# Kernel tuning notes

Measured on AMD Instinct MI355X. Metric: run time of the kernel, lower is better.

Reference implementation:

```python
import jax, jax.numpy as jnp
import numpy as np
from jax import lax

C = 128; HEADS = 16; HD = 8; EPS = 1e-5

def _conv3x3(x, w):
    return lax.conv_general_dilated(x, w, (1, 1), 'SAME', dimension_numbers=('NCHW', 'OIHW', 'NCHW'))

def _cbr3(x, w, g, b):
    # Conv3x3 + BatchNorm(eval, running stats folded -> per-channel affine) + ReLU
    return jax.nn.relu(_conv3x3(x, w) * g[:, None, None] + b[:, None, None])

def _cbr1(x, w, g, b):
    y = jnp.einsum('bchw,oc->bohw', x, w)
    return jax.nn.relu(y * g[:, None, None] + b[:, None, None])

def _ln(t, g, b):
    mu = t.mean(-1, keepdims=True)
    va = ((t - mu) ** 2).mean(-1, keepdims=True)
    return (t - mu) / jnp.sqrt(va + EPS) * g + b

def _gconv1x1(xf, w, b, groups):
    # grouped 1x1 conv on flattened spatial dim: xf [B,Cin,N], w [Cout, Cin//groups]
    B, Cin, N = xf.shape
    Cout = w.shape[0]
    y = jnp.einsum('bgcn,goc->bgon', xf.reshape(B, groups, Cin // groups, N),
                   w.reshape(groups, Cout // groups, Cin // groups))
    return y.reshape(B, Cout, N) + b[:, None]

def _ss_softmax(a):
    # sign * sqrt(|a| + 1e-5) then softmax (GISSA's custom transform)
    a = jnp.sign(a) * jnp.sqrt(jnp.abs(a) + 1e-5)
    return jax.nn.softmax(a, axis=-1)

def _gissa(ximg, qkv_w, qkv_b, g, b, qkv2_w, qkv2_b):
    B, Cc, H, W = ximg.shape
    N = H * W
    xf = ximg.reshape(B, Cc, N)
    qkv = _gconv1x1(xf, qkv_w, qkv_b, HEADS).reshape(B, 3, HEADS, HD, N)
    q, k, v = qkv[:, 0], qkv[:, 1], qkv[:, 2]
    attn = _ss_softmax(jnp.einsum('bhdn,bhen->bhde', q, k) * HD ** -0.5)  # [B,h,hd,hd]
    x1 = jnp.einsum('bhde,bhen->bhdn', attn, v).reshape(B, Cc, N) + xf
    x1 = x1.reshape(B, HEADS, HD, N).transpose(0, 2, 1, 3).reshape(B, Cc, N)  # channel shuffle
    y = x1 * g[:, None] + b[:, None]  # BatchNorm eval affine
    xr = jax.nn.relu(y)
    qkv2 = _gconv1x1(xr, qkv2_w, qkv2_b, HD).reshape(B, 3, HD, HEADS, N)
    q2, k2, v2 = qkv2[:, 0], qkv2[:, 1], qkv2[:, 2]
    attn2 = _ss_softmax(jnp.einsum('bdhn,bdgn->bdhg', q2, k2) * HEADS ** -0.5)  # [B,hd,h,h]
    o = jnp.einsum('bdhg,bdgn->bdhn', attn2, v2).transpose(0, 2, 1, 3).reshape(B, Cc, N) + y
    return o.reshape(B, Cc, H, W)

def _swsa_calc(ximg, pi_w, pi_b, g, b, po_w, po_b):
    B, Cc, H, W = ximg.shape
    t = jnp.einsum('bcn,oc->bon', ximg.reshape(B, Cc, H * W), pi_w) + pi_b[:, None]
    t = t * g[:, None] + b[:, None]  # BN affine
    q = t[:, :Cc].transpose(0, 2, 1)  # [B,N,C]
    v = t[:, Cc:].transpose(0, 2, 1)
    atn = jax.nn.softmax(jnp.einsum('bnc,bmc->bnm', q, q) * Cc ** -0.5, axis=-1)
    y = jnp.einsum('bnm,bmc->bnc', atn, v).transpose(0, 2, 1)  # [B,C,N]
    y = (jnp.einsum('bcn,oc->bon', y, po_w) + po_b[:, None]).reshape(B, Cc, H, W)
    return y, atn

def _swsa_reuse(ximg, atn, pi_w, pi_b, g, b, po_w, po_b):
    B, Cc, H, W = ximg.shape
    t = jnp.einsum('bcn,oc->bon', ximg.reshape(B, Cc, H * W), pi_w) + pi_b[:, None]
    t = t * g[:, None] + b[:, None]
    v = t.transpose(0, 2, 1)
    y = (jnp.einsum('bnm,bmc->bnc', atn, v) * Cc ** -0.5).transpose(0, 2, 1)
    return (jnp.einsum('bcn,oc->bon', y, po_w) + po_b[:, None]).reshape(B, Cc, H, W)

def _forward(x, ssfe_w, ssfe_g, ssfe_b, cc_w, cc_g, cc_b, ln1_g, ln1_b, qkv_w, qkv_b, gbn_g, gbn_b, qkv2_w, qkv2_b, ln2_g, ln2_b, mlp_w1, mlp_b1, mlp_w2, mlp_b2, cs_w, cs_g, cs_b, lfe0_w, lfe0_g, lfe0_b, s0_pi_w, s0_pi_b, s0_bn_g, s0_bn_b, s0_po_w, s0_po_b, lfe1_w, lfe1_g, lfe1_b, s1_pi_w, s1_pi_b, s1_bn_g, s1_bn_b, s1_po_w, s1_po_b, lamuda, fc_w):
    B, Cin, H, W = x.shape
    N = H * W
    # SSFE stem (approximated as Conv3x3+BN+ReLU; source def unavailable)
    xs = _cbr3(x, ssfe_w, ssfe_g, ssfe_b)
    # channel branch: 1x1 CBR + SIT (LN -> GISSA -> residual -> LN -> MLP -> residual)
    xc = _cbr1(xs, cc_w, cc_g, cc_b)
    t = xc.reshape(B, C, N).transpose(0, 2, 1)  # [B,N,C]
    cur = _ln(t, ln1_g, ln1_b).transpose(0, 2, 1).reshape(B, C, H, W)
    t = t + _gissa(cur, qkv_w, qkv_b, gbn_g, gbn_b, qkv2_w, qkv2_b).reshape(B, C, N).transpose(0, 2, 1)
    h = _ln(t, ln2_g, ln2_b)
    h = jax.nn.gelu(h @ mlp_w1.T + mlp_b1, approximate=False) @ mlp_w2.T + mlp_b2
    t = t + h
    xc = t.transpose(0, 2, 1).reshape(B, C, H, W)
    # spatial branch: 3x3 CBR + SCA (LFE + SWSA with attention reuse)
    xp = _cbr3(xs, cs_w, cs_g, cs_b)
    xp = _cbr3(xp, lfe0_w, lfe0_g, lfe0_b) + xp
    y, atn = _swsa_calc(xp, s0_pi_w, s0_pi_b, s0_bn_g, s0_bn_b, s0_po_w, s0_po_b)
    xp = y + xp
    xp = _cbr3(xp, lfe1_w, lfe1_g, lfe1_b) + xp
    xp = _swsa_reuse(xp, atn, s1_pi_w, s1_pi_b, s1_bn_g, s1_bn_b, s1_po_w, s1_po_b) + xp
    lmd = jax.nn.sigmoid(lamuda[0])
    out = lmd * xc + (1.0 - lmd) * xp
    return out.mean(axis=(2, 3)) @ fc_w.T  # global avg pool + fc (dropout p=0 for HUST2013)

def setup_inputs():
    ks = iter(jax.random.split(jax.random.key(0), 64))
    def rn(shape, scale=0.05):
        return jax.random.normal(next(ks), shape, jnp.float32) * scale
    ones = lambda *s: jnp.ones(s, jnp.float32)
    zeros = lambda *s: jnp.zeros(s, jnp.float32)
    return dict(
        x=jax.random.normal(next(ks), (32, 144, 32, 32), jnp.float32),
        ssfe_w=rn((144, 144, 3, 3)), ssfe_g=ones(144), ssfe_b=zeros(144),
        cc_w=rn((128, 144)), cc_g=ones(128), cc_b=zeros(128),
        ln1_g=ones(128), ln1_b=zeros(128),
        qkv_w=rn((384, 8)), qkv_b=zeros(384),
        gbn_g=ones(128), gbn_b=zeros(128),
        qkv2_w=rn((384, 16)), qkv2_b=zeros(384),
        ln2_g=ones(128), ln2_b=zeros(128),
        mlp_w1=rn((512, 128)), mlp_b1=zeros(512),
        mlp_w2=rn((128, 512)), mlp_b2=zeros(128),
        cs_w=rn((128, 144, 3, 3)), cs_g=ones(128), cs_b=zeros(128),
        lfe0_w=rn((128, 128, 3, 3)), lfe0_g=ones(128), lfe0_b=zeros(128),
        s0_pi_w=rn((256, 128)), s0_pi_b=zeros(256), s0_bn_g=ones(256), s0_bn_b=zeros(256),
        s0_po_w=rn((128, 128)), s0_po_b=zeros(128),
        lfe1_w=rn((128, 128, 3, 3)), lfe1_g=ones(128), lfe1_b=zeros(128),
        s1_pi_w=rn((128, 128)), s1_pi_b=zeros(128), s1_bn_g=ones(128), s1_bn_b=zeros(128),
        s1_po_w=rn((128, 128)), s1_po_b=zeros(128),
        lamuda=jnp.full((1,), 0.5, jnp.float32),
        fc_w=rn((16, 128)),
    )

def reference(x, ssfe_w, ssfe_g, ssfe_b, cc_w, cc_g, cc_b, ln1_g, ln1_b, qkv_w, qkv_b, gbn_g, gbn_b, qkv2_w, qkv2_b, ln2_g, ln2_b, mlp_w1, mlp_b1, mlp_w2, mlp_b2, cs_w, cs_g, cs_b, lfe0_w, lfe0_g, lfe0_b, s0_pi_w, s0_pi_b, s0_bn_g, s0_bn_b, s0_po_w, s0_po_b, lfe1_w, lfe1_g, lfe1_b, s1_pi_w, s1_pi_b, s1_bn_g, s1_bn_b, s1_po_w, s1_po_b, lamuda, fc_w):
    return _forward(x, ssfe_w, ssfe_g, ssfe_b, cc_w, cc_g, cc_b, ln1_g, ln1_b, qkv_w, qkv_b, gbn_g, gbn_b, qkv2_w, qkv2_b, ln2_g, ln2_b, mlp_w1, mlp_b1, mlp_w2, mlp_b2, cs_w, cs_g, cs_b, lfe0_w, lfe0_g, lfe0_b, s0_pi_w, s0_pi_b, s0_bn_g, s0_bn_b, s0_po_w, s0_po_b, lfe1_w, lfe1_g, lfe1_b, s1_pi_w, s1_pi_b, s1_bn_g, s1_bn_b, s1_po_w, s1_po_b, lamuda, fc_w)
```

## Files before the change

kernel.cpp:

```cpp
#include <hip/hip_runtime.h>
#include <math.h>


static constexpr int NPIX = 1024;

typedef __attribute__((ext_vector_type(8))) short bf16x8;
typedef __attribute__((ext_vector_type(4))) float f32x4;
typedef __attribute__((ext_vector_type(8))) unsigned short u16x8;
typedef __attribute__((ext_vector_type(4))) unsigned short u16x4;

static __device__ __forceinline__ unsigned short f2bf(float f) {
    unsigned u = __builtin_bit_cast(unsigned, f);
    unsigned r = (u + 0x7fffu + ((u >> 16) & 1u)) >> 16;
    return (unsigned short)r;
}
static __device__ __forceinline__ float bf2f(unsigned short u) {
    unsigned v = ((unsigned)u) << 16;
    return __builtin_bit_cast(float, v);
}

__global__ __launch_bounds__(256) void prepack_convs(
    const float* __restrict__ ssfe_w, const float* __restrict__ cs_w,
    const float* __restrict__ lfe0_w, const float* __restrict__ lfe1_w,
    unsigned short* __restrict__ wssfe, unsigned short* __restrict__ wcs,
// ... 277 lines not shown
    unsigned short* __restrict__ outT,
    const unsigned short* __restrict__ wpi, const float* __restrict__ pi_b,
    const float* __restrict__ pig, const float* __restrict__ pibb,
    unsigned short* __restrict__ qTout, unsigned short* __restrict__ vout)
{
    constexpr int CINP = 128, PITCH = 136, NCHK = 16;
    __shared__ unsigned short X[130 * PITCH];
    unsigned short* Y = X;
    const int tid = threadIdx.x;
    const int b = blockIdx.x, gr = blockIdx.y;
    const int pbase = gr << 6;
    const int gbase = pbase - 33;
    const int wid = tid >> 6, lane = tid & 63;
    const int ll = lane & 15, lq = lane >> 4;
    const int co0w = wid << 5;
    const unsigned short* xb = xT + ((size_t)b << 10) * CINP;

#pragma unroll 1
    for (int idx = tid; idx < 130 * NCHK; idx += 256) {
        const int row = idx / NCHK;
        const int chunk = idx - row * NCHK;
        const int gp = gbase + row;
        u16x8 v = {};
        if (gp >= 0 && gp < 1024)
            v = *(const u16x8*)(xb + (size_t)gp * CINP + chunk * 8);
        *(u16x8*)&X[row * PITCH + chunk * 8] = v;
    }
    __syncthreads();

    f32x4 acc[2][4];
#pragma unroll
    for (int i = 0; i < 2; ++i)
#pragma unroll
        for (int j = 0; j < 4; ++j)
#pragma unroll
            for (int r = 0; r < 4; ++r) acc[i][j][r] = 0.f;

#pragma unroll
    for (int tap = 0; tap < 9; ++tap) {
        const int soff = (tap / 3) * 32 + (tap % 3);
        const int dx = tap % 3;
#pragma unroll
        for (int kc = 0; kc < CINP / 32; ++kc) {
            bf16x8 bfv[4];
#pragma unroll
            for (int j = 0; j < 4; ++j) {
                const int p = j * 16 + ll;
                bf16x8 v = *(const bf16x8*)&X[(p + soff) * PITCH + kc * 32 + lq * 8];
                const bool zed = (dx == 0 && (j & 1) == 0 && ll == 0) ||
                                 (dx == 2 && (j & 1) == 1 && ll == 15);
                if (zed) { bf16x8 z = {}; v = z; }
                bfv[j] = v;
            }
            const unsigned short* wb =
                wrep + ((size_t)tap * 128 + co0w) * CINP + kc * 32 + lq * 8;
#pragma unroll
            for (int i = 0; i < 2; ++i) {
                bf16x8 af = *(const bf16x8*)(wb + (size_t)(i * 16 + ll) * CINP);
#pragma unroll
                for (int j = 0; j < 4; ++j)
                    acc[i][j] = __builtin_amdgcn_mfma_f32_16x16x32_bf16(
                        af, bfv[j], acc[i][j], 0, 0, 0);
            }
        }
    }
    __syncthreads();

#pragma unroll
    for (int i = 0; i < 2; ++i) {
        const int cob = co0w + i * 16 + lq * 4;
        float gv[4], bv[4];
#pragma unroll
        for (int r = 0; r < 4; ++r) { gv[r] = g[cob + r]; bv[r] = bb[cob + r]; }
#pragma unroll
        for (int j = 0; j < 4; ++j) {
            const int pxl = j * 16 + ll;
            const int px = pbase + pxl;
            const size_t rowT = ((size_t)((b << 10) + px)) << 7;
            u16x4 rv = *(const u16x4*)(resT + rowT + cob);
            u16x4 tp;
#pragma unroll
            for (int r = 0; r < 4; ++r) {
                float v = fmaxf(acc[i][j][r] * gv[r] + bv[r], 0.f) + bf2f(rv[r]);
                tp[r] = f2bf(v);
            }
            *(u16x4*)(outT + rowT + cob) = tp;
            const int sw4 = ((pxl >> 2) & 3) << 4;
            *(u16x4*)&Y[pxl * 128 + (cob ^ sw4)] = tp;
        }
    }
    __syncthreads();

    constexpr int NI = PI_COUT / 64;
    const int co0p = wid * (PI_COUT / 4);
    f32x4 acc2[NI][4];
#pragma unroll
    for (int i = 0; i < NI; ++i)
#pragma unroll
        for (int j = 0; j < 4; ++j)
#pragma unroll
            for (int r = 0; r < 4; ++r) acc2[i][j][r] = 0.f;

#pragma unroll
    for (int kk = 0; kk < 4; ++kk) {
        bf16x8 af[NI], bfv[4];
#pragma unroll
        for (int i = 0; i < NI; ++i)
            af[i] = *(const bf16x8*)(wpi + (size_t)(co0p + i * 16 + ll) * 128 + kk * 32 + lq * 8);
#pragma unroll
        for (int j = 0; j < 4; ++j) {
            const int pxl = j * 16 + ll;
            const int sw4 = ((pxl >> 2) & 3) << 4;
            bfv[j] = *(const bf16x8*)&Y[pxl * 128 + ((kk * 32 + lq * 8) ^ sw4)];
        }
#pragma unroll
        for (int i = 0; i < NI; ++i)
#pragma unroll
            for (int j = 0; j < 4; ++j)
                acc2[i][j] = __builtin_amdgcn_mfma_f32_16x16x32_bf16(af[i], bfv[j], acc2[i][j], 0, 0, 0);
    }

#pragma unroll
    for (int i = 0; i < NI; ++i) {
        const int cob = co0p + i * 16 + lq * 4;
        float b0v[4], gv[4], bv[4];
#pragma unroll
        for (int r = 0; r < 4; ++r) {
            b0v[r] = pi_b[cob + r];
            gv[r] = pig[cob + r];
            bv[r] = pibb[cob + r];
        }
#pragma unroll
        for (int j = 0; j < 4; ++j) {
            const int px = pbase + j * 16 + ll;
            float vv[4];
#pragma unroll
            for (int r = 0; r < 4; ++r)
                vv[r] = (acc2[i][j][r] + b0v[r]) * gv[r] + bv[r];
            if (PI_COUT == 256 && cob < 128) {
                u16x4 tp;
#pragma unroll
                for (int r = 0; r < 4; ++r) tp[r] = f2bf(vv[r]);
                *(u16x4*)(qTout + (((size_t)((b << 10) + px)) << 7) + cob) = tp;
            } else {
                const int cv = (PI_COUT == 256) ? cob - 128 : cob;
#pragma unroll
                for (int r = 0; r < 4; ++r)
                    vout[((size_t)(b * 128 + cv + r) << 10) + px] = f2bf(vv[r]);
            }
        }
    }
}

template <int KP>
__global__ __launch_bounds__(256) void lin_mfma_kernel(
    const unsigned short* __restrict__ xT, const unsigned short* __restrict__ wbf,
    const float* __restrict__ bias0, const float* __restrict__ g,
    const float* __restrict__ bb, const unsigned short* __restrict__ resT,
    float* __restrict__ outF, unsigned short* __restrict__ outBF,
    unsigned short* __restrict__ outT, int do_relu)
{
    const int tid = threadIdx.x;
    const int b = blockIdx.x;
    const int n0 = blockIdx.y << 6;
    const int wid = tid >> 6, lane = tid & 63;
    const int ll = lane & 15, lq = lane >> 4;
    const unsigned short* xb = xT + (size_t)((b << 10) + n0) * KP;

    f32x4 acc[2][4];
#pragma unroll
    for (int i = 0; i < 2; ++i)
#pragma unroll
        for (int j = 0; j < 4; ++j)
#pragma unroll
            for (int r = 0; r < 4; ++r) acc[i][j][r] = 0.f;

#pragma unroll
    for (int kk = 0; kk < KP / 32; ++kk) {
        bf16x8 af[2], bfv[4];
#pragma unroll
        for (int i = 0; i < 2; ++i)
            af[i] = *(const bf16x8*)(wbf + (size_t)(wid * 32 + i * 16 + ll) * KP + kk * 32 + lq * 8);
#pragma unroll
        for (int j = 0; j < 4; ++j)
            bfv[j] = *(const bf16x8*)(xb + (size_t)(j * 16 + ll) * KP + kk * 32 + lq * 8);
#pragma unroll
        for (int i = 0; i < 2; ++i)
#pragma unroll
            for (int j = 0; j < 4; ++j)
                acc[i][j] = __builtin_amdgcn_mfma_f32_16x16x32_bf16(af[i], bfv[j], acc[i][j], 0, 0, 0);
    }

#pragma unroll
    for (int i = 0; i < 2; ++i) {
        const int cob = wid * 32 + i * 16 + lq * 4;
        float b0v[4], gv[4], bv[4];
#pragma unroll
        for (int r = 0; r < 4; ++r) {
            b0v[r] = bias0 ? bias0[cob + r] : 0.f;
            gv[r] = g ? g[cob + r] : 1.f;
            bv[r] = g ? bb[cob + r] : 0.f;
        }
#pragma unroll
        for (int j = 0; j < 4; ++j) {
            const int px = n0 + j * 16 + ll;
            const size_t rowT = ((size_t)((b << 10) + px)) << 7;
            u16x4 rv = {};
            if (resT) rv = *(const u16x4*)(resT + rowT + cob);
            u16x4 tp;
#pragma unroll
            for (int r = 0; r < 4; ++r) {
                const int co = cob + r;
                float v = acc[i][j][r] + b0v[r];
                v = v * gv[r] + bv[r];
                if (do_relu) v = fmaxf(v, 0.f);
                if (resT) v += bf2f(rv[r]);
                if (outF) outF[((size_t)((b << 7) + co) << 10) + px] = v;
                unsigned short h = f2bf(v);
                if (outBF) outBF[((size_t)((b << 7) + co) << 10) + px] = h;
                tp[r] = h;
            }
            if (outT) *(u16x4*)(outT + rowT + cob) = tp;
        }
    }
}

__global__ __launch_bounds__(256) void ln_kernel(
    const float* __restrict__ in, const float* __restrict__ g,
    const float* __restrict__ bb, unsigned short* __restrict__ out_bf,
    unsigned short* __restrict__ outT)
{
    const int tid = threadIdx.x;
    const int b = blockIdx.x >> 2;
    const int n = ((blockIdx.x & 3) << 8) + tid;
    const float* ib = in + ((size_t)b << 17) + n;
    float s = 0.f, sq = 0.f;
#pragma unroll 8
    for (int c = 0; c < 128; ++c) {
        float v = ib[(size_t)c << 10];
        s += v;
        sq += v * v;
    }
    const float mu = s * 0.0078125f;
    const float r = rsqrtf(sq * 0.0078125f - mu * mu + 1e-5f);
    unsigned short* obf = out_bf + ((size_t)b << 17) + n;
    unsigned short* oT = outT + (((size_t)b << 10) + n) * 128;
#pragma unroll 2
    for (int c0 = 0; c0 < 128; c0 += 8) {
        u16x8 pk;
#pragma unroll
        for (int e = 0; e < 8; ++e) {
            const int c = c0 + e;
            float v = ib[(size_t)c << 10];
            float y = (v - mu) * r * g[c] + bb[c];
            unsigned short h = f2bf(y);
            obf[(size_t)c << 10] = h;
            pk[e] = h;
        }
        *(u16x8*)(oT + c0) = pk;
    }
}

__global__ __launch_bounds__(256) void gram_kernel(
    const unsigned short* __restrict__ Xbf, float* __restrict__ G)
{
    __shared__ unsigned short Xs[128 * 128];
    const int tid = threadIdx.x;
    const int b = blockIdx.x >> 2;
    const int rg = blockIdx.x & 3;
    const int wid = tid >> 6, lane = tid & 63;
    const int lq = lane >> 4, ll = lane & 15;
    const unsigned short* Xb = Xbf + ((size_t)b << 17);

    f32x4 acc[2][2];
#pragma unroll
    for (int mi = 0; mi < 2; ++mi)
#pragma unroll
        for (int ci = 0; ci < 2; ++ci)
#pragma unroll
            for (int r = 0; r < 4; ++r) acc[mi][ci][r] = 0.f;

#pragma unroll 1
    for (int nt = 0; nt < 8; ++nt) {
        const int n0 = nt << 7;
#pragma unroll
        for (int p = 0; p < 8; ++p) {
            const int ch = (p << 4) + (tid >> 4);
            const int seg = (tid & 15) << 3;
            *(u16x8*)&Xs[ch * 128 + (seg ^ ((ch & 7) << 3))] =
                *(const u16x8*)(Xb + ((size_t)ch << 10) + n0 + seg);
        }
        __syncthreads();
#pragma unroll
        for (int ks = 0; ks < 4; ++ks) {
            bf16x8 af[2], bf_[2];
#pragma unroll
            for (int mi = 0; mi < 2; ++mi) {
                const int ar = (rg << 5) + mi * 16 + ll;
                af[mi] = *(const bf16x8*)&Xs[ar * 128 + ((ks * 32 + lq * 8) ^ ((ar & 7) << 3))];
            }
#pragma unroll
            for (int ci = 0; ci < 2; ++ci) {
                const int br = (wid << 5) + ci * 16 + ll;
                bf_[ci] = *(const bf16x8*)&Xs[br * 128 + ((ks * 32 + lq * 8) ^ ((br & 7) << 3))];
            }
#pragma unroll
            for (int mi = 0; mi < 2; ++mi)
#pragma unroll
                for (int ci = 0; ci < 2; ++ci)
                    acc[mi][ci] = __builtin_amdgcn_mfma_f32_16x16x32_bf16(
                        af[mi], bf_[ci], acc[mi][ci], 0, 0, 0);
        }
        __syncthreads();
    }
    float* Gb = G + ((size_t)b << 14);
#pragma unroll
    for (int mi = 0; mi < 2; ++mi)
#pragma unroll
        for (int ci = 0; ci < 2; ++ci)
#pragma unroll
            for (int r = 0; r < 4; ++r) {
                const int row = (rg << 5) + mi * 16 + lq * 4 + r;
                const int col = (wid << 5) + ci * 16 + ll;
                Gb[row * 128 + col] = acc[mi][ci][r];
            }
}

__global__ __launch_bounds__(256) void sums_kernel(
    const unsigned short* __restrict__ Xbf, float* __restrict__ S)
{
    const int tid = threadIdx.x;
    const int b = blockIdx.x;
    const int ch = tid >> 1, half = tid & 1;
    const unsigned short* p = Xbf + ((size_t)b << 17) + ((size_t)ch << 10) + half * 512;
    float s = 0.f;
#pragma unroll 4
    for (int i = 0; i < 64; ++i) {
        u16x8 v = *(const u16x8*)(p + i * 8);
#pragma unroll
        for (int e = 0; e < 8; ++e) s += bf2f(v[e]);
    }
    s += __shfl_xor(s, 1);
    if (half == 0) S[(b << 7) + ch] = s;
}

__global__ __launch_bounds__(64) void mats1_kernel(
    const float* __restrict__ G, const float* __restrict__ S,
    const float* __restrict__ qkv_w, const float* __restrict__ qkv_b,
    const float* __restrict__ g, const float* __restrict__ bb,
    unsigned short* __restrict__ M1, float* __restrict__ c1)
{
    const int lane = threadIdx.x;
    const int b = blockIdx.x >> 4, h = blockIdx.x & 15;
    const float* Gb = G + ((size_t)b << 14);
    const float* Sb = S + (b << 7);
    const int d = lane >> 3, e = lane & 7;
    const int qch = h * 8 + d, kch = 128 + h * 8 + e;
    const int qoff = (qch / 24) * 8, koff = (kch / 24) * 8;
    float wq[8], wk[8];
#pragma unroll
    for (int i = 0; i < 8; ++i) {
        wq[i] = qkv_w[qch * 8 + i];
        wk[i] = qkv_w[kch * 8 + i];
    }
    float s = 0.f;
#pragma unroll
    for (int i = 0; i < 8; ++i) {
        float gu = 0.f;
#pragma unroll
        for (int j = 0; j < 8; ++j) gu += Gb[(qoff + i) * 128 + koff + j] * wk[j];
        s += wq[i] * gu;
    }
    const float bq = qkv_b[qch], bk = qkv_b[kch];
    float swk = 0.f, swq = 0.f;
#pragma unroll
    for (int j = 0; j < 8; ++j) { swk += wk[j] * Sb[koff + j]; swq += wq[j] * Sb[qoff + j]; }
    s += bq * swk + bk * swq + 1024.f * bq * bk;
    s *= 0.35355339059327373f;
    float a = (s > 0.f) ? sqrtf(s + 1e-5f) : ((s < 0.f) ? -sqrtf(1e-5f - s) : 0.f);
    float mx = a;
    mx = fmaxf(mx, __shfl_xor(mx, 1));
    mx = fmaxf(mx, __shfl_xor(mx, 2));
    mx = fmaxf(mx, __shfl_xor(mx, 4));
    float p = __expf(a - mx);
    float den = p;
    den += __shfl_xor(den, 1);
    den += __shfl_xor(den, 2);
    den += __shfl_xor(den, 4);
    const float A = p / den;

    const int l = e;
    const int cp = d * 16 + h;
    float row[16];
#pragma unroll
    for (int j = 0; j < 16; ++j) row[j] = 0.f;
    float cacc = 0.f;
#pragma unroll
    for (int e2 = 0; e2 < 8; ++e2) {
        const float Ae = __shfl(A, d * 8 + e2);
        const int vch = 256 + h * 8 + e2;
        const int voff = (vch / 24) * 8;
        cacc += Ae * qkv_b[vch];
        if ((voff >> 4) == l) {
            const int base = voff & 15;
#pragma unroll
            for (int j = 0; j < 8; ++j) row[base + j] += Ae * qkv_w[vch * 8 + j];
        }
    }
    const int idc = h * 8 + d;
    if ((idc >> 4) == l) row[idc & 15] += 1.f;
    const float gg = g[cp];
    unsigned short* mrow = M1 + ((size_t)b << 14) + cp * 128 + l * 16;
#pragma unroll
    for (int j = 0; j < 16; ++j) mrow[j] = f2bf(gg * row[j]);
    if (l == 0) c1[(b << 7) + cp] = gg * cacc + bb[cp];
}

__global__ __launch_bounds__(256) void mats2_kernel(
    const float* __restrict__ G, const float* __restrict__ S,
    const float* __restrict__ qkv2_w, const float* __restrict__ qkv2_b,
    unsigned short* __restrict__ M2, float* __restrict__ c2)
{
    const int tid = threadIdx.x;
    const int b = blockIdx.x >> 3, d = blockIdx.x & 7;
    const float* Gb = G + ((size_t)b << 14);
    const float* Sb = S + (b << 7);
    const int h = tid >> 4, gq = tid & 15;
    const int q2ch = d * 16 + h, k2ch = 128 + d * 16 + gq;
    const int qoff = (q2ch / 48) * 16, koff = (k2ch / 48) * 16;
    float wq[16], wk[16];
#pragma unroll
    for (int i = 0; i < 16; ++i) {
        wq[i] = qkv2_w[q2ch * 16 + i];
        wk[i] = qkv2_w[k2ch * 16 + i];
    }
    float s = 0.f;
#pragma unroll
    for (int i = 0; i < 16; ++i) {
        float gu = 0.f;
#pragma unroll
        for (int j = 0; j < 16; ++j) gu += Gb[(qoff + i) * 128 + koff + j] * wk[j];
        s += wq[i] * gu;
    }
    const float bq = qkv2_b[q2ch], bk = qkv2_b[k2ch];
    float swk = 0.f, swq = 0.f;
#pragma unroll
    for (int j = 0; j < 16; ++j) { swk += wk[j] * Sb[koff + j]; swq += wq[j] * Sb[qoff + j]; }
    s += bq * swk + bk * swq + 1024.f * bq * bk;
    s *= 0.25f;
    float a = (s > 0.f) ? sqrtf(s + 1e-5f) : ((s < 0.f) ? -sqrtf(1e-5f - s) : 0.f);
    float mx = a;
    mx = fmaxf(mx, __shfl_xor(mx, 1));
    mx = fmaxf(mx, __shfl_xor(mx, 2));
    mx = fmaxf(mx, __shfl_xor(mx, 4));
    mx = fmaxf(mx, __shfl_xor(mx, 8));
    float p = __expf(a - mx);
    float den = p;
    den += __shfl_xor(den, 1);
    den += __shfl_xor(den, 2);
    den += __shfl_xor(den, 4);
    den += __shfl_xor(den, 8);
    const float A2 = p / den;

    const int l = gq;
    float row[8];
#pragma unroll
    for (int j = 0; j < 8; ++j) row[j] = 0.f;
    float cacc = 0.f;
#pragma unroll
    for (int g2 = 0; g2 < 16; ++g2) {
        const float Ag = __shfl(A2, (tid & 48) + g2);
        const int v2ch = 256 + d * 16 + g2;
        const int voff = (v2ch / 48) * 16;
        cacc += Ag * qkv2_b[v2ch];
        if ((l >> 1) == (voff >> 4)) {
            const int base = (l & 1) * 8;
#pragma unroll
            for (int j = 0; j < 8; ++j) row[j] += Ag * qkv2_w[v2ch * 16 + base + j];
        }
    }
    const int c = h * 8 + d;
    unsigned short* mrow = M2 + ((size_t)b << 14) + c * 128 + l * 8;
#pragma unroll
    for (int j = 0; j < 8; ++j) mrow[j] = f2bf(row[j]);
    if (l == 0) c2[(b << 7) + c] = cacc;
}

__global__ __launch_bounds__(256) void apply1_mfma_kernel(
    const unsigned short* __restrict__ curT, const unsigned short* __restrict__ M1bf,
    const float* __restrict__ c1, float* __restrict__ ybuf,
    unsigned short* __restrict__ yrbf, unsigned short* __restrict__ yrT)
{
    const int tid = threadIdx.x;
    const int b = blockIdx.x >> 3;
    const int n0 = (blockIdx.x & 7) << 7;
    const int wid = tid >> 6, lane = tid & 63;
    const int wr = wid >> 1, wc = wid & 1;
    const int ll = lane & 15, lq = lane >> 4;
    const unsigned short* Mb = M1bf + ((size_t)b << 14);
    const unsigned short* xb = curT + (((size_t)b << 10) + n0 + wc * 64) * 128;

    f32x4 acc[4][4];
#pragma unroll
    for (int i = 0; i < 4; ++i)
#pragma unroll
        for (int j = 0; j < 4; ++j)
#pragma unroll
            for (int r = 0; r < 4; ++r) acc[i][j][r] = 0.f;

#pragma unroll
    for (int kk = 0; kk < 4; ++kk) {
        bf16x8 af[4], bfv[4];
#pragma unroll
        for (int i = 0; i < 4; ++i)
            af[i] = *(const bf16x8*)(Mb + (size_t)(wr * 64 + i * 16 + ll) * 128 + kk * 32 + lq * 8);
#pragma unroll
        for (int j = 0; j < 4; ++j)
            bfv[j] = *(const bf16x8*)(xb + (size_t)(j * 16 + ll) * 128 + kk * 32 + lq * 8);
#pragma unroll
        for (int i = 0; i < 4; ++i)
#pragma unroll
            for (int j = 0; j < 4; ++j)
                acc[i][j] = __builtin_amdgcn_mfma_f32_16x16x32_bf16(af[i], bfv[j], acc[i][j], 0, 0, 0);
    }

#pragma unroll
    for (int i = 0; i < 4; ++i) {
        const int cob = wr * 64 + i * 16 + lq * 4;
        float c1v[4];
#pragma unroll
        for (int r = 0; r < 4; ++r) c1v[r] = c1[(b << 7) + cob + r];
#pragma unroll
        for (int j = 0; j < 4; ++j) {
            const int px = n0 + wc * 64 + j * 16 + ll;
            u16x4 tp;
#pragma unroll
            for (int r = 0; r < 4; ++r) {
                const int co = cob + r;
                const float v = acc[i][j][r] + c1v[r];
                const size_t oi = ((size_t)(b * 128 + co) << 10) + px;
                ybuf[oi] = v;
                const unsigned short h = f2bf(fmaxf(v, 0.f));
                yrbf[oi] = h;
                tp[r] = h;
            }
            *(u16x4*)(yrT + (((size_t)b << 10) + px) * 128 + cob) = tp;
        }
    }
}

__global__ __launch_bounds__(256) void apply2_mfma_kernel(
    const unsigned short* __restrict__ yrT, const unsigned short* __restrict__ M2bf,
    const float* __restrict__ c2, const float* __restrict__ ybuf,
    float* __restrict__ t)
{
    const int tid = threadIdx.x;
    const int b = blockIdx.x >> 3;
    const int n0 = (blockIdx.x & 7) << 7;
    const int wid = tid >> 6, lane = tid & 63;
    const int wr = wid >> 1, wc = wid & 1;
    const int ll = lane & 15, lq = lane >> 4;
    const unsigned short* Mb = M2bf + ((size_t)b << 14);
    const unsigned short* xb = yrT + (((size_t)b << 10) + n0 + wc * 64) * 128;

    f32x4 acc[4][4];
#pragma unroll
    for (int i = 0; i < 4; ++i)
#pragma unroll
        for (int j = 0; j < 4; ++j)
#pragma unroll
            for (int r = 0; r < 4; ++r) acc[i][j][r] = 0.f;

#pragma unroll
    for (int kk = 0; kk < 4; ++kk) {
        bf16x8 af[4], bfv[4];
#pragma unroll
        for (int i = 0; i < 4; ++i)
            af[i] = *(const bf16x8*)(Mb + (size_t)(wr * 64 + i * 16 + ll) * 128 + kk * 32 + lq * 8);
#pragma unroll
        for (int j = 0; j < 4; ++j)
            bfv[j] = *(const bf16x8*)(xb + (size_t)(j * 16 + ll) * 128 + kk * 32 + lq * 8);
#pragma unroll
        for (int i = 0; i < 4; ++i)
#pragma unroll
            for (int j = 0; j < 4; ++j)
                acc[i][j] = __builtin_amdgcn_mfma_f32_16x16x32_bf16(af[i], bfv[j], acc[i][j], 0, 0, 0);
    }

#pragma unroll
    for (int i = 0; i < 4; ++i) {
        const int cob = wr * 64 + i * 16 + lq * 4;
        float c2v[4];
#pragma unroll
        for (int r = 0; r < 4; ++r) c2v[r] = c2[(b << 7) + cob + r];
#pragma unroll
        for (int j = 0; j < 4; ++j) {
            const int px = n0 + wc * 64 + j * 16 + ll;
#pragma unroll
            for (int r = 0; r < 4; ++r) {
                const size_t oi = ((size_t)(b * 128 + cob + r) << 10) + px;
                t[oi] += acc[i][j][r] + c2v[r] + ybuf[oi];
            }
        }
    }
}

__global__ __launch_bounds__(256) void mlp_mfma_kernel(
    float* __restrict__ t, const float* __restrict__ ln_g,
    const float* __restrict__ ln_b, const unsigned short* __restrict__ w1bf,
    const float* __restrict__ b1, const unsigned short* __restrict__ w2bf,
    const float* __restrict__ b2)
{
    __shared__ unsigned char lds[16384 + 65536];
    unsigned char* xnb = lds;
    unsigned char* hb = lds + 16384;

    const int tid = threadIdx.x;
    const int b = blockIdx.x >> 4;
    const int n0 = (blockIdx.x & 15) << 6;
    float* tb = t + ((size_t)b << 17) + n0;

    {
        const int px = tid >> 2, q = tid & 3;
        float v[32];
        float s = 0.f, sq = 0.f;
#pragma unroll
        for (int k = 0; k < 32; ++k) {
            float x = tb[((size_t)(q * 32 + k) << 10) + px];
            v[k] = x;
            s += x;
            sq += x * x;
        }
        s += __shfl_xor(s, 1); s += __shfl_xor(s, 2);
        sq += __shfl_xor(sq, 1); sq += __shfl_xor(sq, 2);
        const float mu = s * 0.0078125f;
        const float rstd = rsqrtf(sq * 0.0078125f - mu * mu + 1e-5f);
        const int sw = (px & 7) << 4;
#pragma unroll
        for (int cc = 0; cc < 4; ++cc) {
            u16x8 pk;
#pragma unroll
            for (int e = 0; e < 8; ++e) {
                int c = q * 32 + cc * 8 + e;
                float xv = (v[cc * 8 + e] - mu) * rstd * ln_g[c] + ln_b[c];
                pk[e] = f2bf(xv);
            }
            *(u16x8*)(xnb + px * 256 + ((q * 64 + cc * 16) ^ sw)) = pk;
        }
    }
    __syncthreads();

    const int wid = tid >> 6, lane = tid & 63;
    const int lr = lane & 15, lk = lane >> 4;

#pragma unroll 1
    for (int pass = 0; pass < 2; ++pass) {
        const int hidbase = (wid << 7) + (pass << 6);
        f32x4 acc[4][4];
#pragma unroll
        for (int i = 0; i < 4; ++i)
#pragma unroll
            for (int j = 0; j < 4; ++j)
#pragma unroll
                for (int r = 0; r < 4; ++r) acc[i][j][r] = 0.f;
#pragma unroll
        for (int kk = 0; kk < 4; ++kk) {
            bf16x8 af[4], bfr[4];
#pragma unroll
            for (int i = 0; i < 4; ++i)
                af[i] = *(const bf16x8*)(w1bf + (size_t)(hidbase + i * 16 + lr) * 128 + kk * 32 + lk * 8);
#pragma unroll
            for (int j = 0; j < 4; ++j) {
                const int px = j * 16 + lr;
                bfr[j] = *(const bf16x8*)(xnb + px * 256 + ((kk * 64 + lk * 16) ^ ((px & 7) << 4)));
            }
#pragma unroll
            for (int i = 0; i < 4; ++i)
#pragma unroll
                for (int j = 0; j < 4; ++j)
                    acc[i][j] = __builtin_amdgcn_mfma_f32_16x16x32_bf16(af[i], bfr[j], acc[i][j], 0, 0, 0);
        }
#pragma unroll
        for (int i = 0; i < 4; ++i) {
            const int hid0 = hidbase + i * 16 + lk * 4;
            float bi[4];
#pragma unroll
            for (int r = 0; r < 4; ++r) bi[r] = b1[hid0 + r];
#pragma unroll
            for (int j = 0; j < 4; ++j) {
                const int px = j * 16 + lr;
                u16x4 pk;
#pragma unroll
                for (int r = 0; r < 4; ++r) {
                    float x = acc[i][j][r] + bi[r];
                    float u = 1.5957691f * x * (1.f + 0.044715f * x * x);
                    float gv = x / (1.f + __expf(-u));
                    pk[r] = f2bf(gv);
                }
                *(u16x4*)(hb + px * 1024 + ((hid0 * 2) ^ ((px & 7) << 4))) = pk;
            }
        }
    }
    __syncthreads();

    f32x4 acc2[2][4];
#pragma unroll
    for (int i = 0; i < 2; ++i)
#pragma unroll
        for (int j = 0; j < 4; ++j)
#pragma unroll
            for (int r = 0; r < 4; ++r) acc2[i][j][r] = 0.f;
#pragma unroll 2
    for (int ks = 0; ks < 16; ++ks) {
        bf16x8 af[2], bfr[4];
#pragma unroll
        for (int i = 0; i < 2; ++i)
            af[i] = *(const bf16x8*)(w2bf + (size_t)((wid << 5) + i * 16 + lr) * 512 + ks * 32 + lk * 8);
#pragma unroll
        for (int j = 0; j < 4; ++j) {
            const int px = j * 16 + lr;
            bfr[j] = *(const bf16x8*)(hb + px * 1024 + ((ks * 64 + lk * 16) ^ ((px & 7) << 4)));
        }
#pragma unroll
        for (int i = 0; i < 2; ++i)
#pragma unroll
            for (int j = 0; j < 4; ++j)
                acc2[i][j] = __builtin_amdgcn_mfma_f32_16x16x32_bf16(af[i], bfr[j], acc2[i][j], 0, 0, 0);
    }
#pragma unroll
    for (int i = 0; i < 2; ++i) {
        const int cb = (wid << 5) + i * 16 + lk * 4;
        float b2v[4];
#pragma unroll
        for (int r = 0; r < 4; ++r) b2v[r] = b2[cb + r];
#pragma unroll
        for (int j = 0; j < 4; ++j) {
            const int px = j * 16 + lr;
#pragma unroll
            for (int r = 0; r < 4; ++r) {
                const size_t off = ((size_t)(cb + r) << 10) + px;
                tb[off] += acc2[i][j][r] + b2v[r];
            }
        }
    }
}

template <int REUSE>
__global__ __launch_bounds__(256) void swsa_po_kernel(
    const unsigned short* __restrict__ qT, const unsigned short* __restrict__ vbf,
    const unsigned short* __restrict__ wpo, const float* __restrict__ po_b,
    const unsigned short* __restrict__ resT,
    unsigned short* __restrict__ outT, float* __restrict__ outF, float fscale,
    float* __restrict__ statsM, float* __restrict__ statsL)
{
// ... 185 lines not shown
        for (int j = 0; j < 4; ++j)
#pragma unroll
            for (int r = 0; r < 4; ++r) acc2[i][j][r] = 0.f;
#pragma unroll
    for (int kk = 0; kk < 4; ++kk) {
        bf16x8 af[2], bfv[4];
#pragma unroll
        for (int i = 0; i < 2; ++i)
            af[i] = *(const bf16x8*)(wpo + (size_t)(wid * 32 + i * 16 + ll) * 128 + kk * 32 + lq * 8);
#pragma unroll
        for (int j = 0; j < 4; ++j) {
            const int row = j * 16 + ll;
            const int sw4 = ((row >> 2) & 3) << 4;
            bfv[j] = *(const bf16x8*)&K_lds[row * 128 + ((kk * 32 + lq * 8) ^ sw4)];
        }
#pragma unroll
        for (int i = 0; i < 2; ++i)
#pragma unroll
            for (int j = 0; j < 4; ++j)
                acc2[i][j] = __builtin_amdgcn_mfma_f32_16x16x32_bf16(af[i], bfv[j], acc2[i][j], 0, 0, 0);
    }

#pragma unroll
    for (int i = 0; i < 2; ++i) {
        const int cob = wid * 32 + i * 16 + lq * 4;
        float pob[4];
#pragma unroll
        for (int r = 0; r < 4; ++r) pob[r] = po_b[cob + r];
#pragma unroll
        for (int j = 0; j < 4; ++j) {
            const int px = n0 + j * 16 + ll;
            const size_t rowT = ((size_t)((b << 10) + px)) << 7;
            u16x4 rv = *(const u16x4*)(resT + rowT + cob);
            float vv[4];
#pragma unroll
            for (int r = 0; r < 4; ++r)
                vv[r] = acc2[i][j][r] + pob[r] + bf2f(rv[r]);
            if (outT) {
                u16x4 tp;
#pragma unroll
                for (int r = 0; r < 4; ++r) tp[r] = f2bf(vv[r]);
                *(u16x4*)(outT + rowT + cob) = tp;
            }
            if (outF) {
#pragma unroll
                for (int r = 0; r < 4; ++r)
                    outF[((size_t)(b * 128 + cob + r) << 10) + px] = vv[r];
            }
        }
    }
}

__global__ __launch_bounds__(256) void mean_kernel(
    const float* __restrict__ xc, const float* __restrict__ xp,
    const float* __restrict__ lamuda, float* __restrict__ meanb)
{
    const int wid = threadIdx.x >> 6, lane = threadIdx.x & 63;
    const int row = (blockIdx.x << 2) + wid;
    const float lmd = 1.f / (1.f + __expf(-lamuda[0]));
    const float* a = xc + ((size_t)row << 10) + (lane << 2);
    const float* d = xp + ((size_t)row << 10) + (lane << 2);
    float s = 0.f;
#pragma unroll
    for (int i = 0; i < 4; ++i) {
        float4 va = *(const float4*)(a + (i << 8));
        float4 vd = *(const float4*)(d + (i << 8));
        s += lmd * (va.x + va.y + va.z + va.w) +
             (1.f - lmd) * (vd.x + vd.y + vd.z + vd.w);
    }
#pragma unroll
    for (int o = 1; o < 64; o <<= 1) s += __shfl_xor(s, o);
    if (lane == 0) meanb[row] = s * (1.f / 1024.f);
}

__global__ __launch_bounds__(256) void fc_kernel(
    const float* __restrict__ meanb, const float* __restrict__ fc_w,
    float* __restrict__ outp)
{
    const int idx = blockIdx.x * 256 + threadIdx.x;
    if (idx >= 512) return;
    const int b = idx >> 4, o = idx & 15;
    float s = 0.f;
#pragma unroll 4
    for (int c = 0; c < 128; ++c) s += fc_w[o * 128 + c] * meanb[b * 128 + c];
    outp[b * 16 + o] = s;
}

extern "C" void kernel_launch(void* const* d_in, const int* in_sizes, int n_in,
                              void* d_out, int out_size, void* d_ws, size_t ws_size,
                              hipStream_t stream)
{
    (void)in_sizes; (void)n_in; (void)out_size; (void)ws_size;

    const float* x       = (const float*)d_in[0];
    const float* ssfe_w  = (const float*)d_in[1];
    const float* ssfe_g  = (const float*)d_in[2];
    const float* ssfe_b  = (const float*)d_in[3];
    const float* cc_w    = (const float*)d_in[4];
    const float* cc_g    = (const float*)d_in[5];
    const float* cc_b    = (const float*)d_in[6];
    const float* ln1_g   = (const float*)d_in[7];
    const float* ln1_b   = (const float*)d_in[8];
    const float* qkv_w   = (const float*)d_in[9];
    const float* qkv_b   = (const float*)d_in[10];
    const float* gbn_g   = (const float*)d_in[11];
    const float* gbn_b   = (const float*)d_in[12];
    const float* qkv2_w  = (const float*)d_in[13];
    const float* qkv2_b  = (const float*)d_in[14];
    const float* ln2_g   = (const float*)d_in[15];
    const float* ln2_b   = (const float*)d_in[16];
    const float* mlp_w1  = (const float*)d_in[17];
    const float* mlp_b1  = (const float*)d_in[18];
    const float* mlp_w2  = (const float*)d_in[19];
    const float* mlp_b2  = (const float*)d_in[20];
    const float* cs_w    = (const float*)d_in[21];
    const float* cs_g    = (const float*)d_in[22];
    const float* cs_b    = (const float*)d_in[23];
    const float* lfe0_w  = (const float*)d_in[24];
    const float* lfe0_g  = (const float*)d_in[25];
    const float* lfe0_b  = (const float*)d_in[26];
    const float* s0_pi_w = (const float*)d_in[27];
    const float* s0_pi_b = (const float*)d_in[28];
    const float* s0_bn_g = (const float*)d_in[29];
    const float* s0_bn_b = (const float*)d_in[30];
    const float* s0_po_w = (const float*)d_in[31];
    const float* s0_po_b = (const float*)d_in[32];
    const float* lfe1_w  = (const float*)d_in[33];
    const float* lfe1_g  = (const float*)d_in[34];
    const float* lfe1_b  = (const float*)d_in[35];
    const float* s1_pi_w = (const float*)d_in[36];
    const float* s1_pi_b = (const float*)d_in[37];
    const float* s1_bn_g = (const float*)d_in[38];
    const float* s1_bn_b = (const float*)d_in[39];
    const float* s1_po_w = (const float*)d_in[40];
    const float* s1_po_b = (const float*)d_in[41];
    const float* lamuda  = (const float*)d_in[42];
    const float* fc_w    = (const float*)d_in[43];
    float* out = (float*)d_out;
    float* ws = (float*)d_ws;

    float* xs = ws;
    float* t  = ws + 4718592;
    float* Qr = ws + 13107200;
    float* P2 = ws + 25690112;
    float* P3 = ws + 29884416;

    unsigned short* xT0 = (unsigned short*)Qr;

    unsigned short* curbf = (unsigned short*)Qr;
    unsigned short* curT  = (unsigned short*)(Qr + 2097152);
    unsigned short* yrbf  = (unsigned short*)(Qr + 4194304);
    unsigned short* yrT   = (unsigned short*)(Qr + 6291456);
    unsigned short* xsT   = (unsigned short*)(Qr + 8388608);
    float* ybuf = P2;

    unsigned short* xpT   = (unsigned short*)Qr;
    unsigned short* v0    = (unsigned short*)(Qr + 2097152);
    unsigned short* v1    = (unsigned short*)(Qr + 4194304);
    unsigned short* xp3T  = (unsigned short*)(Qr + 6291456);
    unsigned short* xp2T  = (unsigned short*)(Qr + 8388608);
    unsigned short* xp4T  = (unsigned short*)(Qr + 8388608);
    unsigned short* qT0   = (unsigned short*)P2;

    unsigned short* linw  = (unsigned short*)(Qr + 11010048);
    unsigned short* wcc   = linw;
    unsigned short* wpi0  = linw + 20480;
    unsigned short* wpi1  = linw + 53248;
    unsigned short* wpo0  = linw + 69632;
    unsigned short* wpo1  = linw + 86016;
    unsigned short* w1bf  = linw + 102400;
    unsigned short* w2bf  = linw + 167936;
    float* meanb  = Qr + 11200000;
    float* statsM = Qr + 11204096;
    float* statsL = Qr + 11236864;

    float* Gbuf  = P3 + 1048576;
    float* Sbuf  = P3 + 1572864;
    unsigned short* M1bf = (unsigned short*)(P3 + 1576960);
    float* c1buf = P3 + 1839104;
    unsigned short* M2bf = (unsigned short*)(P3 + 1843200);
    float* c2buf = P3 + 2105344;

    unsigned short* wssfe = (unsigned short*)P3;
    unsigned short* wcs   = (unsigned short*)(P3 + 131072);
    unsigned short* wlfe0 = (unsigned short*)(P3 + 262144);
    unsigned short* wlfe1 = (unsigned short*)xs;

    const dim3 blk(256);

    prepack_convs<<<dim3((686592 + 255) / 256), blk, 0, stream>>>(
        ssfe_w, cs_w, lfe0_w, lfe1_w, wssfe, wcs, wlfe0, wlfe1);
    prepack_lins<<<dim3((233472 + 255) / 256), blk, 0, stream>>>(
        cc_w, s0_pi_w, s1_pi_w, s0_po_w, s1_po_w, mlp_w1, mlp_w2, linw);

    cvt_xT_kernel<<<dim3(32, 16), blk, 0, stream>>>(x, xT0);
    conv3x3_ssfe_kernel<<<dim3(32, 16), blk, 0, stream>>>(
        xT0, wssfe, ssfe_g, ssfe_b, xsT);
    lin_mfma_kernel<160><<<dim3(32, 16), blk, 0, stream>>>(
        xsT, wcc, nullptr, cc_g, cc_b, nullptr, t, nullptr, nullptr, 1);

    ln_kernel<<<dim3(128), blk, 0, stream>>>(t, ln1_g, ln1_b, curbf, curT);
    gram_kernel<<<dim3(128), blk, 0, stream>>>(curbf, Gbuf);
    sums_kernel<<<dim3(32), blk, 0, stream>>>(curbf, Sbuf);
    mats1_kernel<<<dim3(512), dim3(64), 0, stream>>>(Gbuf, Sbuf, qkv_w, qkv_b, gbn_g, gbn_b, M1bf, c1buf);
    apply1_mfma_kernel<<<dim3(256), blk, 0, stream>>>(curT, M1bf, c1buf, ybuf, yrbf, yrT);
    gram_kernel<<<dim3(128), blk, 0, stream>>>(yrbf, Gbuf);
    sums_kernel<<<dim3(32), blk, 0, stream>>>(yrbf, Sbuf);
    mats2_kernel<<<dim3(256), blk, 0, stream>>>(Gbuf, Sbuf, qkv2_w, qkv2_b, M2bf, c2buf);
    apply2_mfma_kernel<<<dim3(256), blk, 0, stream>>>(yrT, M2bf, c2buf, ybuf, t);

    mlp_mfma_kernel<<<dim3(512), blk, 0, stream>>>(t, ln2_g, ln2_b, w1bf, mlp_b1, w2bf, mlp_b2);

    conv3x3_lds_kernel<160><<<dim3(32, 16), blk, 0, stream>>>(
        xsT, wcs, cs_g, cs_b, nullptr, xpT, 128);
    conv3x3_pi_kernel<256><<<dim3(32, 16), blk, 0, stream>>>(
        xpT, wlfe0, lfe0_g, lfe0_b, xpT, xp2T,
        wpi0, s0_pi_b, s0_bn_g, s0_bn_b, qT0, v0);
    swsa_po_kernel<0><<<dim3(512), blk, 0, stream>>>(
        qT0, v0, wpo0, s0_po_b, xp2T, xp3T, nullptr, 1.0f, statsM, statsL);
    conv3x3_pi_kernel<128><<<dim3(32, 16), blk, 0, stream>>>(
        xp3T, wlfe1, lfe1_g, lfe1_b, xp3T, xp4T,
        wpi1, s1_pi_b, s1_bn_g, s1_bn_b, nullptr, v1);
    swsa_po_kernel<1><<<dim3(512), blk, 0, stream>>>(
        qT0, v1, wpo1, s1_po_b, xp4T, nullptr, P3, 0.08838834764831845f, statsM, statsL);

    mean_kernel<<<dim3(1024), blk, 0, stream>>>(t, P3, lamuda, meanb);
    fc_kernel<<<dim3(2), blk, 0, stream>>>(meanb, fc_w, out);
}
```

Baseline: 423.6 us.

## Fuse channel-combine linear with LayerNorm, merge gram and sums kernels, store residual in bf16

The cc 1x1 linear kernel now computes LayerNorm statistics per pixel in-block through shared-memory partial sums and writes the normalized bf16 outputs directly, which removes the separate ln_kernel and its re-read of t. The gram and channel-sum kernels are merged into a single launch with extra blocks for the sums, cutting two launches. The intermediate ybuf residual is stored as bf16 instead of fp32, halving that traffic at the cost of some precision in the residual add.

```diff
diff --git a/kernel.cpp b/kernel.cpp
--- a/kernel.cpp
+++ b/kernel.cpp
@@ -453,20 +453,21 @@
     }
 }
 
-template <int KP>
-__global__ __launch_bounds__(256) void lin_mfma_kernel(
+__global__ __launch_bounds__(256) void cc_ln_kernel(
     const unsigned short* __restrict__ xT, const unsigned short* __restrict__ wbf,
-    const float* __restrict__ bias0, const float* __restrict__ g,
-    const float* __restrict__ bb, const unsigned short* __restrict__ resT,
-    float* __restrict__ outF, unsigned short* __restrict__ outBF,
-    unsigned short* __restrict__ outT, int do_relu)
-{
+    const float* __restrict__ g, const float* __restrict__ bb,
+    const float* __restrict__ ln_g, const float* __restrict__ ln_b,
+    float* __restrict__ t, unsigned short* __restrict__ out_bf,
+    unsigned short* __restrict__ outT)
+{
+    __shared__ float Ssum[4][64];
+    __shared__ float Ssq[4][64];
     const int tid = threadIdx.x;
     const int b = blockIdx.x;
     const int n0 = blockIdx.y << 6;
     const int wid = tid >> 6, lane = tid & 63;
     const int ll = lane & 15, lq = lane >> 4;
-    const unsigned short* xb = xT + (size_t)((b << 10) + n0) * KP;
+    const unsigned short* xb = xT + (size_t)((b << 10) + n0) * 160;
 
     f32x4 acc[2][4];
 #pragma unroll
@@ -477,14 +478,14 @@
             for (int r = 0; r < 4; ++r) acc[i][j][r] = 0.f;
 
 #pragma unroll
-    for (int kk = 0; kk < KP / 32; ++kk) {
+    for (int kk = 0; kk < 5; ++kk) {
         bf16x8 af[2], bfv[4];
 #pragma unroll
         for (int i = 0; i < 2; ++i)
-            af[i] = *(const bf16x8*)(wbf + (size_t)(wid * 32 + i * 16 + ll) * KP + kk * 32 + lq * 8);
+            af[i] = *(const bf16x8*)(wbf + (size_t)(wid * 32 + i * 16 + ll) * 160 + kk * 32 + lq * 8);
 #pragma unroll
         for (int j = 0; j < 4; ++j)
-            bfv[j] = *(const bf16x8*)(xb + (size_t)(j * 16 + ll) * KP + kk * 32 + lq * 8);
+            bfv[j] = *(const bf16x8*)(xb + (size_t)(j * 16 + ll) * 160 + kk * 32 + lq * 8);
 #pragma unroll
         for (int i = 0; i < 2; ++i)
 #pragma unroll
@@ -492,81 +493,97 @@
                 acc[i][j] = __builtin_amdgcn_mfma_f32_16x16x32_bf16(af[i], bfv[j], acc[i][j], 0, 0, 0);
     }
 
+    float vv[2][4][4];
+    float sj[4] = {0.f, 0.f, 0.f, 0.f};
+    float sqj[4] = {0.f, 0.f, 0.f, 0.f};
 #pragma unroll
     for (int i = 0; i < 2; ++i) {
         const int cob = wid * 32 + i * 16 + lq * 4;
-        float b0v[4], gv[4], bv[4];
-#pragma unroll
-        for (int r = 0; r < 4; ++r) {
-            b0v[r] = bias0 ? bias0[cob + r] : 0.f;
-            gv[r] = g ? g[cob + r] : 1.f;
-            bv[r] = g ? bb[cob + r] : 0.f;
-        }
+        float gv[4], bv[4];
+#pragma unroll
+        for (int r = 0; r < 4; ++r) { gv[r] = g[cob + r]; bv[r] = bb[cob + r]; }
 #pragma unroll
         for (int j = 0; j < 4; ++j) {
             const int px = n0 + j * 16 + ll;
-            const size_t rowT = ((size_t)((b << 10) + px)) << 7;
-            u16x4 rv = {};
-            if (resT) rv = *(const u16x4*)(resT + rowT + cob);
+#pragma unroll
+            for (int r = 0; r < 4; ++r) {
+                const float val = fmaxf(acc[i][j][r] * gv[r] + bv[r], 0.f);
+                vv[i][j][r] = val;
+                t[((size_t)((b << 7) + cob + r) << 10) + px] = val;
+                sj[j] += val;
+                sqj[j] += val * val;
+            }
+        }
+    }
+#pragma unroll
+    for (int j = 0; j < 4; ++j) {
+        sj[j] += __shfl_xor(sj[j], 16);
+        sj[j] += __shfl_xor(sj[j], 32);
+        sqj[j] += __shfl_xor(sqj[j], 16);
+        sqj[j] += __shfl_xor(sqj[j], 32);
+    }
+    if (lq == 0) {
+#pragma unroll
+        for (int j = 0; j < 4; ++j) {
+            Ssum[wid][j * 16 + ll] = sj[j];
+            Ssq[wid][j * 16 + ll] = sqj[j];
+        }
+    }
+    __syncthreads();
+
+    float mu[4], rst[4];
+#pragma unroll
+    for (int j = 0; j < 4; ++j) {
+        const int p = j * 16 + ll;
+        const float s = Ssum[0][p] + Ssum[1][p] + Ssum[2][p] + Ssum[3][p];
+        const float sq = Ssq[0][p] + Ssq[1][p] + Ssq[2][p] + Ssq[3][p];
+        mu[j] = s * 0.0078125f;
+        rst[j] = rsqrtf(sq * 0.0078125f - mu[j] * mu[j] + 1e-5f);
+    }
+
+#pragma unroll
+    for (int i = 0; i < 2; ++i) {
+        const int cob = wid * 32 + i * 16 + lq * 4;
+        float lg[4], lb[4];
+#pragma unroll
+        for (int r = 0; r < 4; ++r) { lg[r] = ln_g[cob + r]; lb[r] = ln_b[cob + r]; }
+#pragma unroll
+        for (int j = 0; j < 4; ++j) {
+            const int px = n0 + j * 16 + ll;
             u16x4 tp;
 #pragma unroll
             for (int r = 0; r < 4; ++r) {
-                const int co = cob + r;
-                float v = acc[i][j][r] + b0v[r];
-                v = v * gv[r] + bv[r];
-                if (do_relu) v = fmaxf(v, 0.f);
-                if (resT) v += bf2f(rv[r]);
-                if (outF) outF[((size_t)((b << 7) + co) << 10) + px] = v;
-                unsigned short h = f2bf(v);
-                if (outBF) outBF[((size_t)((b << 7) + co) << 10) + px] = h;
+                const float y = (vv[i][j][r] - mu[j]) * rst[j] * lg[r] + lb[r];
+                const unsigned short h = f2bf(y);
+                out_bf[((size_t)((b << 7) + cob + r) << 10) + px] = h;
                 tp[r] = h;
             }
-            if (outT) *(u16x4*)(outT + rowT + cob) = tp;
-        }
-    }
-}
-
-__global__ __launch_bounds__(256) void ln_kernel(
-    const float* __restrict__ in, const float* __restrict__ g,
-    const float* __restrict__ bb, unsigned short* __restrict__ out_bf,
-    unsigned short* __restrict__ outT)
-{
-    const int tid = threadIdx.x;
-    const int b = blockIdx.x >> 2;
-    const int n = ((blockIdx.x & 3) << 8) + tid;
-    const float* ib = in + ((size_t)b << 17) + n;
-    float s = 0.f, sq = 0.f;
-#pragma unroll 8
-    for (int c = 0; c < 128; ++c) {
-        float v = ib[(size_t)c << 10];
-        s += v;
-        sq += v * v;
-    }
-    const float mu = s * 0.0078125f;
-    const float r = rsqrtf(sq * 0.0078125f - mu * mu + 1e-5f);
-    unsigned short* obf = out_bf + ((size_t)b << 17) + n;
-    unsigned short* oT = outT + (((size_t)b << 10) + n) * 128;
-#pragma unroll 2
-    for (int c0 = 0; c0 < 128; c0 += 8) {
-        u16x8 pk;
-#pragma unroll
-        for (int e = 0; e < 8; ++e) {
-            const int c = c0 + e;
-            float v = ib[(size_t)c << 10];
-            float y = (v - mu) * r * g[c] + bb[c];
-            unsigned short h = f2bf(y);
-            obf[(size_t)c << 10] = h;
-            pk[e] = h;
-        }
-        *(u16x8*)(oT + c0) = pk;
-    }
-}
-
-__global__ __launch_bounds__(256) void gram_kernel(
-    const unsigned short* __restrict__ Xbf, float* __restrict__ G)
+            *(u16x4*)(outT + (((size_t)((b << 10) + px)) << 7) + cob) = tp;
+        }
+    }
+}
+
+__global__ __launch_bounds__(256) void gram_sums_kernel(
+    const unsigned short* __restrict__ Xbf, float* __restrict__ G,
+    float* __restrict__ S)
 {
     __shared__ unsigned short Xs[128 * 128];
     const int tid = threadIdx.x;
+    if (blockIdx.x >= 128) {
+        const int b = blockIdx.x - 128;
+        const int ch = tid >> 1, half = tid & 1;
+        const unsigned short* p = Xbf + ((size_t)b << 17) + ((size_t)ch << 10) + half * 512;
+        float s = 0.f;
+#pragma unroll 4
+        for (int i = 0; i < 64; ++i) {
+            u16x8 v = *(const u16x8*)(p + i * 8);
+#pragma unroll
+            for (int e = 0; e < 8; ++e) s += bf2f(v[e]);
+        }
+        s += __shfl_xor(s, 1);
+        if (half == 0) S[(b << 7) + ch] = s;
+        return;
+    }
     const int b = blockIdx.x >> 2;
     const int rg = blockIdx.x & 3;
     const int wid = tid >> 6, lane = tid & 63;
@@ -625,24 +642,6 @@
                 const int col = (wid << 5) + ci * 16 + ll;
                 Gb[row * 128 + col] = acc[mi][ci][r];
             }
-}
-
-__global__ __launch_bounds__(256) void sums_kernel(
-    const unsigned short* __restrict__ Xbf, float* __restrict__ S)
-{
-    const int tid = threadIdx.x;
-    const int b = blockIdx.x;
-    const int ch = tid >> 1, half = tid & 1;
-    const unsigned short* p = Xbf + ((size_t)b << 17) + ((size_t)ch << 10) + half * 512;
-    float s = 0.f;
-#pragma unroll 4
-    for (int i = 0; i < 64; ++i) {
-        u16x8 v = *(const u16x8*)(p + i * 8);
-#pragma unroll
-        for (int e = 0; e < 8; ++e) s += bf2f(v[e]);
-    }
-    s += __shfl_xor(s, 1);
-    if (half == 0) S[(b << 7) + ch] = s;
 }
 
 __global__ __launch_bounds__(64) void mats1_kernel(
@@ -789,7 +788,7 @@
 
 __global__ __launch_bounds__(256) void apply1_mfma_kernel(
     const unsigned short* __restrict__ curT, const unsigned short* __restrict__ M1bf,
-    const float* __restrict__ c1, float* __restrict__ ybuf,
+    const float* __restrict__ c1, unsigned short* __restrict__ ybufb,
     unsigned short* __restrict__ yrbf, unsigned short* __restrict__ yrT)
 {
     const int tid = threadIdx.x;
@@ -840,7 +839,7 @@
                 const int co = cob + r;
                 const float v = acc[i][j][r] + c1v[r];
                 const size_t oi = ((size_t)(b * 128 + co) << 10) + px;
-                ybuf[oi] = v;
+                ybufb[oi] = f2bf(v);
                 const unsigned short h = f2bf(fmaxf(v, 0.f));
                 yrbf[oi] = h;
                 tp[r] = h;
@@ -852,7 +851,7 @@
 
 __global__ __launch_bounds__(256) void apply2_mfma_kernel(
     const unsigned short* __restrict__ yrT, const unsigned short* __restrict__ M2bf,
-    const float* __restrict__ c2, const float* __restrict__ ybuf,
+    const float* __restrict__ c2, const unsigned short* __restrict__ ybufb,
     float* __restrict__ t)
 {
     const int tid = threadIdx.x;
@@ -900,7 +899,7 @@
 #pragma unroll
             for (int r = 0; r < 4; ++r) {
                 const size_t oi = ((size_t)(b * 128 + cob + r) << 10) + px;
-                t[oi] += acc[i][j][r] + c2v[r] + ybuf[oi];
+                t[oi] += acc[i][j][r] + c2v[r] + bf2f(ybufb[oi]);
             }
         }
     }
@@ -1392,7 +1391,7 @@
     unsigned short* yrbf  = (unsigned short*)(Qr + 4194304);
     unsigned short* yrT   = (unsigned short*)(Qr + 6291456);
     unsigned short* xsT   = (unsigned short*)(Qr + 8388608);
-    float* ybuf = P2;
+    unsigned short* ybufb = (unsigned short*)P2;
 
     unsigned short* xpT   = (unsigned short*)Qr;
     unsigned short* v0    = (unsigned short*)(Qr + 2097152);
@@ -1436,18 +1435,16 @@
     cvt_xT_kernel<<<dim3(32, 16), blk, 0, stream>>>(x, xT0);
     conv3x3_ssfe_kernel<<<dim3(32, 16), blk, 0, stream>>>(
         xT0, wssfe, ssfe_g, ssfe_b, xsT);
-    lin_mfma_kernel<160><<<dim3(32, 16), blk, 0, stream>>>(
-        xsT, wcc, nullptr, cc_g, cc_b, nullptr, t, nullptr, nullptr, 1);
-
-    ln_kernel<<<dim3(128), blk, 0, stream>>>(t, ln1_g, ln1_b, curbf, curT);
-    gram_kernel<<<dim3(128), blk, 0, stream>>>(curbf, Gbuf);
-    sums_kernel<<<dim3(32), blk, 0, stream>>>(curbf, Sbuf);
+
+    cc_ln_kernel<<<dim3(32, 16), blk, 0, stream>>>(
+        xsT, wcc, cc_g, cc_b, ln1_g, ln1_b, t, curbf, curT);
+
+    gram_sums_kernel<<<dim3(160), blk, 0, stream>>>(curbf, Gbuf, Sbuf);
     mats1_kernel<<<dim3(512), dim3(64), 0, stream>>>(Gbuf, Sbuf, qkv_w, qkv_b, gbn_g, gbn_b, M1bf, c1buf);
-    apply1_mfma_kernel<<<dim3(256), blk, 0, stream>>>(curT, M1bf, c1buf, ybuf, yrbf, yrT);
-    gram_kernel<<<dim3(128), blk, 0, stream>>>(yrbf, Gbuf);
-    sums_kernel<<<dim3(32), blk, 0, stream>>>(yrbf, Sbuf);
+    apply1_mfma_kernel<<<dim3(256), blk, 0, stream>>>(curT, M1bf, c1buf, ybufb, yrbf, yrT);
+    gram_sums_kernel<<<dim3(160), blk, 0, stream>>>(yrbf, Gbuf, Sbuf);
     mats2_kernel<<<dim3(256), blk, 0, stream>>>(Gbuf, Sbuf, qkv2_w, qkv2_b, M2bf, c2buf);
-    apply2_mfma_kernel<<<dim3(256), blk, 0, stream>>>(yrT, M2bf, c2buf, ybuf, t);
+    apply2_mfma_kernel<<<dim3(256), blk, 0, stream>>>(yrT, M2bf, c2buf, ybufb, t);
 
     mlp_mfma_kernel<<<dim3(512), blk, 0, stream>>>(t, ln2_g, ln2_b, w1bf, mlp_b1, w2bf, mlp_b2);
 
```

Result: faster. 391.5 us (-7.6%).
